# Optimization experiments

Hardware: AMD Instinct MI355X
Metric: run time of the kernel (lower is better)

Reference implementation:

```python
import jax, jax.numpy as jnp
import numpy as np

B, L, DIM, ET, NH, SD, NC = 32, 200, 36, 128, 64, 9, 2


def setup_inputs() -> dict:
    key = jax.random.key(0)
    ks = jax.random.split(key, 16)
    f = jnp.float32
    vals = jax.random.normal(ks[0], (B, L, DIM), f)
    obs = (jax.random.uniform(ks[1], (B, L, DIM)) < 0.7).astype(f)  # 0/1 observation mask
    x = jnp.concatenate([vals, obs], -1)                            # (B, L, 2*DIM)
    time_steps = jnp.sort(jax.random.uniform(ks[2], (B, L)), axis=1)
    static_info = jax.random.normal(ks[3], (B, SD), f)
    query_param = jnp.linspace(0.0, 1.0, ET, dtype=f)               # nn.Parameter(linspace)

    def lin(k, o, i, s):
        return jax.random.normal(k, (o, i), f) * s

    return dict(
        x=x, time_steps=time_steps, static_info=static_info, query_param=query_param,
        periodic_w=lin(ks[4], ET - 1, 1, 1.0), periodic_b=jnp.zeros((ET - 1,), f),
        timelin_w=lin(ks[5], 1, 1, 1.0), timelin_b=jnp.zeros((1,), f),
        qw=lin(ks[6], ET, ET, ET ** -0.5), qb=jnp.zeros((ET,), f),
        kw=lin(ks[7], ET, ET, ET ** -0.5), kb=jnp.zeros((ET,), f),
        ow=lin(ks[8], DIM, 2 * DIM, (2 * DIM) ** -0.5), ob=jnp.zeros((DIM,), f),
        gru_w_ih=lin(ks[9], 3 * NH, DIM, DIM ** -0.5),
        gru_w_hh=lin(ks[10], 3 * NH, NH, NH ** -0.5),
        gru_b_ih=jnp.zeros((3 * NH,), f), gru_b_hh=jnp.zeros((3 * NH,), f),
        st_w=lin(ks[11], 8, SD, SD ** -0.5), st_b=jnp.zeros((8,), f),
        c1_w=lin(ks[12], NH + 8, NH + 8, (NH + 8) ** -0.5), c1_b=jnp.zeros((NH + 8,), f),
        bn_g=jnp.ones((NH + 8,), f), bn_b=jnp.zeros((NH + 8,), f),
        c2_w=lin(ks[13], NC, NH + 8, (NH + 8) ** -0.5), c2_b=jnp.zeros((NC,), f),
        rand_mask=jax.random.randint(ks[14], (B, L), 0, 2, jnp.int32),
    )


def reference(x, time_steps, static_info, query_param, periodic_w, periodic_b,
              timelin_w, timelin_b, qw, qb, kw, kb, ow, ob,
              gru_w_ih, gru_w_hh, gru_b_ih, gru_b_hh, st_w, st_b,
              c1_w, c1_b, bn_g, bn_b, c2_w, c2_b, rand_mask):
    dim = x.shape[-1] // 2
    irr = x[:, :, dim:]                                   # observation mask channels
    temp = rand_mask.astype(x.dtype)[:, :, None]          # random_masking keep-mask
    m_small = irr * temp
    irr2 = jnp.concatenate([irr, irr], -1)                # (B, L, 2*dim)
    m2 = jnp.concatenate([m_small, m_small], -1)

    def time_emb(tt):
        tt = tt[..., None]
        return jnp.concatenate([tt @ timelin_w.T + timelin_b,
                                jnp.sin(tt @ periodic_w.T + periodic_b)], -1)

    key_e = time_emb(time_steps)                          # (B, L, ET)
    query_e = time_emb(query_param[None, :])[0]           # (ET, ET)
    q = query_e @ qw.T + qb                               # num_heads=1 => dk=ET
    k = key_e @ kw.T + kb
    scores = jnp.einsum('qd,bld->bql', q, k) / jnp.sqrt(jnp.asarray(ET, x.dtype))

    def mta(mask):
        # per-channel masked softmax over keys l: (B, Lq, L, 2*dim)
        s5 = jnp.where(mask[:, None, :, :] == 0, jnp.asarray(-1e9, x.dtype),
                       scores[:, :, :, None])
        p = jax.nn.softmax(s5, axis=2)
        o = jnp.einsum('bqld,bld->bqd', p, x)             # (B, Lq, 2*dim)
        return o @ ow.T + ob                              # (B, Lq, dim)

    out_te = mta(irr2)
    out1_te = mta(m2)

    sx = x[:, :, :dim]
    sx_g = jnp.round(jax.nn.sigmoid(jnp.einsum('bld,ble->bde', sx, sx)))
    sout = jax.nn.sigmoid(jnp.einsum('bqd,bqe->bde', out_te, out_te))

    def step(h, xt):  # torch GRU cell, gate order r,z,n
        gi = xt @ gru_w_ih.T + gru_b_ih
        gh = h @ gru_w_hh.T + gru_b_hh
        ir, iz, inn = jnp.split(gi, 3, -1)
        hr, hz, hn = jnp.split(gh, 3, -1)
        r = jax.nn.sigmoid(ir + hr)
        z = jax.nn.sigmoid(iz + hz)
        n = jnp.tanh(inn + r * hn)
        return (1 - z) * n + z * h, None

    h0 = jnp.zeros((x.shape[0], gru_w_hh.shape[1]), x.dtype)
    h_fin, _ = jax.lax.scan(step, h0, jnp.swapaxes(out_te, 0, 1))

    st = static_info @ st_w.T + st_b
    cls_in = jnp.concatenate([h_fin, st], 1)
    z1 = cls_in @ c1_w.T + c1_b
    mu = z1.mean(0)
    var = z1.var(0)                                       # BatchNorm1d (training stats)
    zn = (z1 - mu) / jnp.sqrt(var + 1e-5) * bn_g + bn_b
    zg = jax.nn.gelu(zn, approximate=False)
    logits = zg @ c2_w.T + c2_b
    return (out_te, out1_te, logits, sx_g, sout, query_param)
```

## Files before the change

### kernel.cpp

```cpp
#include <hip/hip_runtime.h>

#define B_   32
#define L_   200
#define DIM_ 36
#define ET_  128
#define NH_  64
#define SD_  9
#define NC_  2

#define O_TE   0
#define O_T1   147456
#define O_LG   294912
#define O_SXG  294976
#define O_SOUT 336448
#define O_QP   377920

typedef __fp16 half_t;
typedef __attribute__((ext_vector_type(2))) __fp16 half2_t;

__device__ __forceinline__ float sigm(float x) { return 1.f / (1.f + expf(-x)); }
__device__ __forceinline__ float fsigm(float x) {
  return __builtin_amdgcn_rcpf(1.f + __expf(-x));
}
__device__ __forceinline__ float ftanh(float x) {
  return 2.f * __builtin_amdgcn_rcpf(1.f + __expf(-2.f * x)) - 1.f;
}
__device__ __forceinline__ half2_t f2h2(float a, float b) {
  return __builtin_amdgcn_cvt_pkrtz(a, b);
}
__device__ __forceinline__ float dot2acc(half2_t w, half2_t h, float acc) {
#if __has_builtin(__builtin_amdgcn_fdot2)
  return __builtin_amdgcn_fdot2(w, h, acc, false);
#else
  return acc + (float)w.x * (float)h.x + (float)w.y * (float)h.y;
#endif
}

__global__ __launch_bounds__(256) void k_pre2(
    const float* __restrict__ qw, const float* __restrict__ kw,
    const float* __restrict__ qb, const float* __restrict__ qp,
    const float* __restrict__ pw, const float* __restrict__ pb,
    const float* __restrict__ tlw, const float* __restrict__ tlb,
    const float* __restrict__ x, float* __restrict__ qm2,
    float* __restrict__ xmean, float* __restrict__ out) {
  int blk = blockIdx.x, t = threadIdx.x;
  if (blk < 128) {
    __shared__ float eq[128];
    __shared__ float uq[128];
    int q = blk;
    if (t < 128) {
      float tt = qp[q];
      eq[t] = (t == 0) ? tt * tlw[0] + tlb[0]
                       : __sinf(tt * pw[t - 1] + pb[t - 1]);
    }
    __syncthreads();
    if (t < 128) {
      const float4* qw4 = (const float4*)(qw + (size_t)t * 128);
      float a = qb[t];
      #pragma unroll 8
      for (int c = 0; c < 32; c++) {
        float4 w = qw4[c];
        a += eq[4 * c] * w.x + eq[4 * c + 1] * w.y +
             eq[4 * c + 2] * w.z + eq[4 * c + 3] * w.w;
      }
      uq[t] = a;
    }
    __syncthreads();
    if (t < 128) {
      float a = 0.f;
      #pragma unroll 8
      for (int i = 0; i < 128; i++) a += uq[i] * kw[i * 128 + t];
      qm2[q * 128 + t] = a * 0.088388347648318447f;
      if (q == 0) out[O_QP + t] = qp[t];
    }
    return;
  }
  int b = blk - 128;
  if (t < 72) {
    float s = 0.f;
    const float* xb = x + (size_t)b * L_ * 72 + t;
    #pragma unroll 8
    for (int l = 0; l < L_; l++) s += xb[(size_t)l * 72];
    xmean[b * 72 + t] = s * (1.0f / L_);
  }
}

__global__ __launch_bounds__(1024, 1) void k_attn(
    const float* __restrict__ qm, const float* __restrict__ ts,
    const float* __restrict__ pw, const float* __restrict__ pb,
    const float* __restrict__ tlw, const float* __restrict__ tlb,
    const float* __restrict__ x, const int* __restrict__ rm,
    const float* __restrict__ xmean, const float* __restrict__ ow,
    const float* __restrict__ ob, float* __restrict__ out) {
  __shared__ __align__(16) char Abuf[103936];
  __shared__ __align__(16) float qs[16][128];
  __shared__ __align__(16) float sc[16][200];
  __shared__ __align__(16) float owsh[DIM_][72];
  float*   ksA  = (float*)Abuf;
  half2_t* wsh2 = (half2_t*)Abuf;
  float*   sums = (float*)(Abuf + 57600);
  float*   ofr  = (float*)(Abuf + 57600 + 36864);

  int b = blockIdx.x >> 3;
  int q0 = (blockIdx.x & 7) << 4;
  int tid = threadIdx.x;

  const float4* qsrc = (const float4*)(qm + q0 * ET_);
  for (int i = tid; i < 16 * 32; i += 1024) ((float4*)qs)[i] = qsrc[i];
  const float4* owsrc = (const float4*)ow;
  for (int i = tid; i < DIM_ * 18; i += 1024) ((float4*)owsh)[i] = owsrc[i];
  {
    float tl_w = tlw[0], tl_b = tlb[0];
    const float* tsb = ts + b * L_;
    for (int i = tid; i < L_ * 128; i += 1024) {
      int l = i >> 7, j = i & 127;
      float t = tsb[l];
      float e = (j == 0) ? t * tl_w + tl_b : __sinf(t * pw[j - 1] + pb[j - 1]);
      int blkj = (j >> 2) ^ ((l >> 2) & 7);
      ksA[(l << 7) + (blkj << 2) + (j & 3)] = e;
    }
  }
  __syncthreads();

  {
    int w = tid >> 6, lg = tid & 63;
    int qp2 = w >> 1;
    int lh = w & 1;
    float acc[2][2];
    #pragma unroll
    for (int i = 0; i < 2; i++)
      #pragma unroll
      for (int j = 0; j < 2; j++) acc[i][j] = 0.f;
    const float4* ks4 = (const float4*)ksA;
    const float4* qs4 = (const float4*)qs;
    int lbase = 100 * lh + 2 * lg;
    int swz0 = (lbase >> 2) & 7;
    int swz1 = ((lbase + 1) >> 2) & 7;
    #pragma unroll 4
    for (int d4 = 0; d4 < 32; d4++) {
      float4 kv[2];
      {
        int l0c = (lbase < 100 * lh + 100) ? lbase : (100 * lh + 99);
        int l1c = (lbase + 1 < 100 * lh + 100) ? lbase + 1 : (100 * lh + 99);
        kv[0] = ks4[(l0c << 5) + (d4 ^ swz0)];
        kv[1] = ks4[(l1c << 5) + (d4 ^ swz1)];
      }
      #pragma unroll
      for (int i = 0; i < 2; i++) {
        float4 qv = qs4[(2 * qp2 + i) * 32 + d4];
        #pragma unroll
        for (int j = 0; j < 2; j++)
          acc[i][j] += qv.x * kv[j].x + qv.y * kv[j].y +
                       qv.z * kv[j].z + qv.w * kv[j].w;
      }
    }
    if (2 * lg < 100) {
      #pragma unroll
      for (int i = 0; i < 2; i++) {
        float2 v = {acc[i][0], acc[i][1]};
        *((float2*)(&sc[2 * qp2 + i][lbase])) = v;
      }
    }
  }
  __syncthreads();

  {
    int qi = tid >> 6, li = tid & 63;
    float m = -1e30f;
    for (int l = li; l < L_; l += 64) m = fmaxf(m, sc[qi][l]);
    #pragma unroll
    for (int off = 32; off >= 1; off >>= 1) m = fmaxf(m, __shfl_xor(m, off));
    for (int l = li; l < L_; l += 64) sc[qi][l] = __expf(sc[qi][l] - m);
  }

  {
    const float2* xb2 = (const float2*)(x + (size_t)b * L_ * 72);
    const int* rmb = rm + b * L_;
    for (int i = tid; i < L_ * 72; i += 1024) {
      int l = i / 72, c2 = i % 72;
      int seg = c2 / 18, fh = c2 % 18;
      float2 v = xb2[l * 36 + fh];
      float2 o = xb2[l * 36 + 18 + fh];
      float rr = (float)rmb[l];
      float w0, w1;
      if (seg == 0)      { w0 = o.x * v.x;      w1 = o.y * v.y; }
      else if (seg == 1) { w0 = o.x;            w1 = o.y; }
      else if (seg == 2) { w0 = o.x * v.x * rr; w1 = o.y * v.y * rr; }
      else               { w0 = o.x * rr;       w1 = o.y * rr; }
      wsh2[l * 72 + c2] = f2h2(w0, w1);
    }
  }
  __syncthreads();

  {
    int quarter = tid >> 8, tt = tid & 255;
    int qi = tt >> 4, li = tt & 15;
    int l0 = quarter * 50;
    float accA[8], accB[8];
    #pragma unroll
    for (int k = 0; k < 8; k++) { accA[k] = 0.f; accB[k] = 0.f; }
    const float4* wA = (const float4*)wsh2;
    #pragma unroll 2
    for (int l = l0; l < l0 + 50; l++) {
      float ev = sc[qi][l];
      float4 wa = wA[l * 18 + li];
      union { float f; half2_t h; } u0, u1, u2, u3;
      u0.f = wa.x; u1.f = wa.y; u2.f = wa.z; u3.f = wa.w;
      accA[0] += ev * (float)u0.h.x; accA[1] += ev * (float)u0.h.y;
      accA[2] += ev * (float)u1.h.x; accA[3] += ev * (float)u1.h.y;
      accA[4] += ev * (float)u2.h.x; accA[5] += ev * (float)u2.h.y;
      accA[6] += ev * (float)u3.h.x; accA[7] += ev * (float)u3.h.y;
      if (li < 2) {
        float4 wb = wA[l * 18 + 16 + li];
        union { float f; half2_t h; } b0, b1, b2, b3;
        b0.f = wb.x; b1.f = wb.y; b2.f = wb.z; b3.f = wb.w;
        accB[0] += ev * (float)b0.h.x; accB[1] += ev * (float)b0.h.y;
        accB[2] += ev * (float)b1.h.x; accB[3] += ev * (float)b1.h.y;
        accB[4] += ev * (float)b2.h.x; accB[5] += ev * (float)b2.h.y;
        accB[6] += ev * (float)b3.h.x; accB[7] += ev * (float)b3.h.y;
      }
    }
    float* sq = sums + quarter * 2304 + qi * 144;
    float4* sA = (float4*)(sq + 8 * li);
    sA[0] = make_float4(accA[0], accA[1], accA[2], accA[3]);
    sA[1] = make_float4(accA[4], accA[5], accA[6], accA[7]);
    if (li < 2) {
      float4* sB = (float4*)(sq + 128 + 8 * li);
      sB[0] = make_float4(accB[0], accB[1], accB[2], accB[3]);
      sB[1] = make_float4(accB[4], accB[5], accB[6], accB[7]);
    }
  }
  __syncthreads();

  const float* xm = xmean + b * 72;
  for (int idx = tid; idx < 16 * DIM_; idx += 1024) {
    int qq = idx / DIM_, j = idx % DIM_;
    const float* s0 = sums + qq * 144;
    const float* s1 = s0 + 2304;
    const float* s2 = s1 + 2304;
    const float* s3 = s2 + 2304;
    float numA = (s0[j] + s1[j]) + (s2[j] + s3[j]);
    float denA = (s0[36 + j] + s1[36 + j]) + (s2[36 + j] + s3[36 + j]);
    float numB = (s0[72 + j] + s1[72 + j]) + (s2[72 + j] + s3[72 + j]);
    float denB = (s0[108 + j] + s1[108 + j]) + (s2[108 + j] + s3[108 + j]);
    float al, ah, bl, bh;
    if (denA > 0.f) { al = numA / denA; ah = 1.f; }
    else            { al = xm[j];       ah = xm[36 + j]; }
    if (denB > 0.f) { bl = numB / denB; bh = 1.f; }
    else            { bl = xm[j];       bh = xm[36 + j]; }
    float* oq = ofr + qq * 144;
    oq[j] = al;      oq[36 + j] = ah;
    oq[72 + j] = bl; oq[108 + j] = bh;
  }
  __syncthreads();

  for (int idx = tid; idx < 16 * 72; idx += 1024) {
    int qq = idx / 72, t = idx % 72;
    int v = t / DIM_, i2 = t % DIM_;
    const float4* o4 = (const float4*)(ofr + qq * 144 + v * 72);
    const float4* w4 = (const float4*)(owsh[i2]);
    float a = ob[i2];
    #pragma unroll
    for (int d4 = 0; d4 < 18; d4++) {
      float4 ov = o4[d4], wv = w4[d4];
      a += ov.x * wv.x + ov.y * wv.y + ov.z * wv.z + ov.w * wv.w;
    }
    size_t off = ((size_t)b * ET_ + q0 + qq) * DIM_ + i2;
    out[(v == 0 ? O_TE : O_T1) + off] = a;
  }
}

__global__ __launch_bounds__(256, 1) void k_sg(
    const float* __restrict__ out_ro, const float* __restrict__ x,
    const float* __restrict__ wih, const float* __restrict__ bih,
    const float* __restrict__ whh, const float* __restrict__ bhh,
    float* __restrict__ hfin, float* __restrict__ out) {
  __shared__ __align__(16) float ote_s[ET_][DIM_];
  __shared__ float gis[ET_][3 * NH_];
  __shared__ __align__(16) half2_t hpk[NH_ / 2];
  int blk = blockIdx.x, t = threadIdx.x;

  if (blk < 32) {
    int b = blk;
    float* sxs = (float*)gis;
    const float4* osrc = (const float4*)(out_ro + O_TE + (size_t)b * ET_ * DIM_);
    for (int idx = t; idx < ET_ * 9; idx += 256)
      ((float4*)&ote_s[0][0])[idx] = osrc[idx];
    const float4* xsrc = (const float4*)(x + (size_t)b * L_ * 72);
    for (int idx = t; idx < L_ * 18; idx += 256) {
      int l = idx / 18, c = idx % 18;
      ((float4*)&sxs[l * 76])[c] = xsrc[idx];
    }
    __syncthreads();
    for (int idx = t; idx < DIM_ * DIM_; idx += 256) {
      int d = idx / DIM_, e = idx % DIM_;
      float s = 0.f;
      #pragma unroll 8
      for (int q = 0; q < ET_; q++) s += ote_s[q][d] * ote_s[q][e];
      out[O_SOUT + (size_t)b * DIM_ * DIM_ + idx] = sigm(s);
    }
    for (int idx = t; idx < DIM_ * DIM_; idx += 256) {
      int d = idx / DIM_, e = idx % DIM_;
      float s = 0.f;
      #pragma unroll 8
      for (int l = 0; l < L_; l++) s += sxs[l * 76 + d] * sxs[l * 76 + e];
      out[O_SXG + (size_t)b * DIM_ * DIM_ + idx] = rintf(sigm(s));
    }
    return;
  }

  int b = blk - 32;
  const float* ote = out_ro + O_TE;
  const float4* osrc = (const float4*)(ote + (size_t)b * ET_ * DIM_);
  for (int idx = t; idx < ET_ * DIM_ / 4; idx += 256)
    ((float4*)&ote_s[0][0])[idx] = osrc[idx];
  __syncthreads();

  if (t < 3 * NH_) {
    float wv[DIM_];
    const float* wrow = wih + (size_t)t * DIM_;
    #pragma unroll
    for (int d = 0; d < DIM_; d++) wv[d] = wrow[d];
    float bi = bih[t] + ((t < 2 * NH_) ? bhh[t] : 0.f);
    for (int q = 0; q < ET_; q++) {
      const float4* xr = (const float4*)ote_s[q];
      float a = bi;
      #pragma unroll
      for (int c = 0; c < 9; c++) {
        float4 xv = xr[c];
        a += xv.x * wv[4 * c] + xv.y * wv[4 * c + 1] +
             xv.z * wv[4 * c + 2] + xv.w * wv[4 * c + 3];
      }
      gis[q][t] = a;
    }
  }
  __syncthreads();
  if (t >= 64) return;

  half2_t wr[32], wz[32], wn[32];
  {
    const float2* r0 = (const float2*)(whh + (size_t)t * NH_);
    const float2* r1 = (const float2*)(whh + (size_t)(NH_ + t) * NH_);
    const float2* r2 = (const float2*)(whh + (size_t)(2 * NH_ + t) * NH_);
    #pragma unroll
    for (int c = 0; c < 32; c++) {
      float2 a = r0[c], bb = r1[c], cc = r2[c];
      wr[c] = f2h2(a.x, a.y);
      wz[c] = f2h2(bb.x, bb.y);
      wn[c] = f2h2(cc.x, cc.y);
    }
  }
  float bh_n = bhh[2 * NH_ + t];

  float h = 0.f;
  ((half_t*)hpk)[t] = (half_t)0.f;
  for (int q = 0; q < ET_; q++) {
    float gi_r = gis[q][t];
    float gi_z = gis[q][NH_ + t];
    float gi_n = gis[q][2 * NH_ + t];
    float ar = 0.f, az = 0.f, an = 0.f;
    const float4* hp4 = (const float4*)hpk;
    #pragma unroll
    for (int c4 = 0; c4 < 8; c4++) {
      float4 hv = hp4[c4];
      union { float f; half2_t h; } u0, u1, u2, u3;
      u0.f = hv.x; u1.f = hv.y; u2.f = hv.z; u3.f = hv.w;
      int c = c4 * 4;
      ar = dot2acc(wr[c + 0], u0.h, ar);
      az = dot2acc(wz[c + 0], u0.h, az);
      an = dot2acc(wn[c + 0], u0.h, an);
      ar = dot2acc(wr[c + 1], u1.h, ar);
      az = dot2acc(wz[c + 1], u1.h, az);
      an = dot2acc(wn[c + 1], u1.h, an);
      ar = dot2acc(wr[c + 2], u2.h, ar);
      az = dot2acc(wz[c + 2], u2.h, az);
      an = dot2acc(wn[c + 2], u2.h, an);
      ar = dot2acc(wr[c + 3], u3.h, ar);
      az = dot2acc(wz[c + 3], u3.h, az);
      an = dot2acc(wn[c + 3], u3.h, an);
    }
    float r = fsigm(gi_r + ar);
    float z = fsigm(gi_z + az);
    float n = ftanh(gi_n + r * (an + bh_n));
    h = n + z * (h - n);
    ((half_t*)hpk)[t] = (half_t)h;
  }
  hfin[b * NH_ + t] = h;
}

__global__ __launch_bounds__(256) void k_cls(
    const float* __restrict__ hfin, const float* __restrict__ si,
    const float* __restrict__ stw, const float* __restrict__ stb,
    const float* __restrict__ c1w, const float* __restrict__ c1b,
    const float* __restrict__ bng, const float* __restrict__ bnb,
    const float* __restrict__ c2w, const float* __restrict__ c2b,
    float* __restrict__ out) {
  __shared__ float cin[B_][72];
  __shared__ float z1[B_][72];
  __shared__ float zg[B_][72];
  int t = threadIdx.x;
  for (int idx = t; idx < B_ * 8; idx += 256) {
    int b = idx / 8, j = idx % 8;
    float acc = stb[j];
    #pragma unroll
    for (int d = 0; d < SD_; d++) acc += si[b * SD_ + d] * stw[j * SD_ + d];
    cin[b][NH_ + j] = acc;
  }
  for (int idx = t; idx < B_ * NH_; idx += 256)
    cin[idx / NH_][idx % NH_] = hfin[idx];
  __syncthreads();
  for (int idx = t; idx < B_ * 72; idx += 256) {
    int b = idx / 72, j = idx % 72;
    float acc = c1b[j];
    #pragma unroll 8
    for (int d = 0; d < 72; d++) acc += cin[b][d] * c1w[j * 72 + d];
    z1[b][j] = acc;
  }
  __syncthreads();
  if (t < 72) {
    float mu = 0.f;
    for (int b = 0; b < B_; b++) mu += z1[b][t];
    mu *= (1.f / B_);
    float vv = 0.f;
    for (int b = 0; b < B_; b++) { float d = z1[b][t] - mu; vv += d * d; }
    vv *= (1.f / B_);
    float inv = 1.f / sqrtf(vv + 1e-5f);
    float g = bng[t], bb = bnb[t];
    for (int b = 0; b < B_; b++) {
      float zn = (z1[b][t] - mu) * inv * g + bb;
      zg[b][t] = 0.5f * zn * (1.f + erff(zn * 0.70710678118654752f));
    }
  }
  __syncthreads();
  for (int idx = t; idx < B_ * NC_; idx += 256) {
    int b = idx / NC_, c = idx % NC_;
    float acc = c2b[c];
    #pragma unroll 8
    for (int d = 0; d < 72; d++) acc += zg[b][d] * c2w[c * 72 + d];
    out[O_LG + idx] = acc;
  }
}

extern "C" void kernel_launch(void* const* d_in, const int* in_sizes, int n_in,
                              void* d_out, int out_size, void* d_ws,
                              size_t ws_size, hipStream_t stream) {
  const float* x    = (const float*)d_in[0];
  const float* ts   = (const float*)d_in[1];
  const float* si   = (const float*)d_in[2];
  const float* qp   = (const float*)d_in[3];
  const float* pw   = (const float*)d_in[4];
  const float* pb   = (const float*)d_in[5];
  const float* tlw  = (const float*)d_in[6];
  const float* tlb  = (const float*)d_in[7];
  const float* qw   = (const float*)d_in[8];
  const float* qb   = (const float*)d_in[9];
  const float* kw   = (const float*)d_in[10];
  const float* ow   = (const float*)d_in[12];
  const float* ob   = (const float*)d_in[13];
  const float* wih  = (const float*)d_in[14];
  const float* whh  = (const float*)d_in[15];
  const float* bih  = (const float*)d_in[16];
  const float* bhh  = (const float*)d_in[17];
  const float* stw  = (const float*)d_in[18];
  const float* stb  = (const float*)d_in[19];
  const float* c1w  = (const float*)d_in[20];
  const float* c1b  = (const float*)d_in[21];
  const float* bng  = (const float*)d_in[22];
  const float* bnb  = (const float*)d_in[23];
  const float* c2w  = (const float*)d_in[24];
  const float* c2b  = (const float*)d_in[25];
  const int*   rm   = (const int*)d_in[26];

  float* out = (float*)d_out;

  float* W = (float*)d_ws;
  float* ws_qm2   = W;
  float* ws_xmean = W + 16384;
  float* ws_hfin  = W + 18688;

  hipLaunchKernelGGL(k_pre2, dim3(160), dim3(256), 0, stream,
                     qw, kw, qb, qp, pw, pb, tlw, tlb, x, ws_qm2, ws_xmean,
                     out);
  hipLaunchKernelGGL(k_attn, dim3(B_ * 8), dim3(1024), 0, stream,
                     ws_qm2, ts, pw, pb, tlw, tlb, x, rm, ws_xmean, ow, ob,
                     out);
  hipLaunchKernelGGL(k_sg, dim3(64), dim3(256), 0, stream,
                     out, x, wih, bih, whh, bhh, ws_hfin, out);
  hipLaunchKernelGGL(k_cls, dim3(1), dim3(256), 0, stream,
                     ws_hfin, si, stw, stb, c1w, c1b, bng, bnb, c2w, c2b,
                     out);
}
```

Measured before the change: 231.1 us.

## Fuse attention, GRU, Gram and classifier kernels into one persistent megakernel

Result: slower. 305.2 us (+32.1%).

```diff
diff --git a/kernel.cpp b/kernel.cpp
--- a/kernel.cpp
+++ b/kernel.cpp
@@ -42,8 +42,10 @@
     const float* __restrict__ pw, const float* __restrict__ pb,
     const float* __restrict__ tlw, const float* __restrict__ tlb,
     const float* __restrict__ x, float* __restrict__ qm2,
-    float* __restrict__ xmean, float* __restrict__ out) {
+    float* __restrict__ xmean, int* __restrict__ cnt,
+    float* __restrict__ out) {
   int blk = blockIdx.x, t = threadIdx.x;
+  if (blk == 0 && t >= 128 && t < 128 + 33) cnt[t - 128] = 0;
   if (blk < 128) {
     __shared__ float eq[128];
     __shared__ float uq[128];
@@ -85,359 +87,385 @@
   }
 }
 
-__global__ __launch_bounds__(1024, 1) void k_attn(
+__global__ __launch_bounds__(1024, 1) void k_mega(
     const float* __restrict__ qm, const float* __restrict__ ts,
     const float* __restrict__ pw, const float* __restrict__ pb,
     const float* __restrict__ tlw, const float* __restrict__ tlb,
     const float* __restrict__ x, const int* __restrict__ rm,
     const float* __restrict__ xmean, const float* __restrict__ ow,
-    const float* __restrict__ ob, float* __restrict__ out) {
-  __shared__ __align__(16) char Abuf[103936];
-  __shared__ __align__(16) float qs[16][128];
-  __shared__ __align__(16) float sc[16][200];
-  __shared__ __align__(16) float owsh[DIM_][72];
-  float*   ksA  = (float*)Abuf;
-  half2_t* wsh2 = (half2_t*)Abuf;
-  float*   sums = (float*)(Abuf + 57600);
-  float*   ofr  = (float*)(Abuf + 57600 + 36864);
-
-  int b = blockIdx.x >> 3;
-  int q0 = (blockIdx.x & 7) << 4;
-  int tid = threadIdx.x;
-
-  const float4* qsrc = (const float4*)(qm + q0 * ET_);
-  for (int i = tid; i < 16 * 32; i += 1024) ((float4*)qs)[i] = qsrc[i];
-  const float4* owsrc = (const float4*)ow;
-  for (int i = tid; i < DIM_ * 18; i += 1024) ((float4*)owsh)[i] = owsrc[i];
-  {
-    float tl_w = tlw[0], tl_b = tlb[0];
-    const float* tsb = ts + b * L_;
-    for (int i = tid; i < L_ * 128; i += 1024) {
-      int l = i >> 7, j = i & 127;
-      float t = tsb[l];
-      float e = (j == 0) ? t * tl_w + tl_b : __sinf(t * pw[j - 1] + pb[j - 1]);
-      int blkj = (j >> 2) ^ ((l >> 2) & 7);
-      ksA[(l << 7) + (blkj << 2) + (j & 3)] = e;
-    }
+    const float* __restrict__ ob, const float* __restrict__ wih,
+    const float* __restrict__ bih, const float* __restrict__ whh,
+    const float* __restrict__ bhh, const float* __restrict__ si,
+    const float* __restrict__ stw, const float* __restrict__ stb,
+    const float* __restrict__ c1w, const float* __restrict__ c1b,
+    const float* __restrict__ bng, const float* __restrict__ bnb,
+    const float* __restrict__ c2w, const float* __restrict__ c2b,
+    float* __restrict__ hfin, int* __restrict__ cnt,
+    float* __restrict__ out) {
+  __shared__ __align__(16) char SMEM[135296];
+  int blk = blockIdx.x, tid = threadIdx.x;
+
+  if (blk < 256) {
+    float*   ksA  = (float*)SMEM;
+    half2_t* wsh2 = (half2_t*)SMEM;
+    float*   sums = (float*)(SMEM + 57600);
+    float*   ofr  = (float*)(SMEM + 57600 + 36864);
+    float (*qs)[128]  = (float(*)[128])(SMEM + 103936);
+    float (*sc)[200]  = (float(*)[200])(SMEM + 112128);
+    float (*owsh)[72] = (float(*)[72])(SMEM + 124928);
+
+    int b = blk >> 3;
+    int q0 = (blk & 7) << 4;
+
+    const float4* qsrc = (const float4*)(qm + q0 * ET_);
+    for (int i = tid; i < 16 * 32; i += 1024) ((float4*)qs)[i] = qsrc[i];
+    const float4* owsrc = (const float4*)ow;
+    for (int i = tid; i < DIM_ * 18; i += 1024) ((float4*)owsh)[i] = owsrc[i];
+    {
+      float tl_w = tlw[0], tl_b = tlb[0];
+      const float* tsb = ts + b * L_;
+      for (int i = tid; i < L_ * 128; i += 1024) {
+        int l = i >> 7, j = i & 127;
+        float t = tsb[l];
+        float e = (j == 0) ? t * tl_w + tl_b
+                           : __sinf(t * pw[j - 1] + pb[j - 1]);
+        int blkj = (j >> 2) ^ ((l >> 2) & 7);
+        ksA[(l << 7) + (blkj << 2) + (j & 3)] = e;
+      }
+    }
+    __syncthreads();
+
+    {
+      int w = tid >> 6, lg = tid & 63;
+      int qp2 = w >> 1, lh = w & 1;
+      float acc[2][2];
+      #pragma unroll
+      for (int i = 0; i < 2; i++)
+        #pragma unroll
+        for (int j = 0; j < 2; j++) acc[i][j] = 0.f;
+      const float4* ks4 = (const float4*)ksA;
+      const float4* qs4 = (const float4*)qs;
+      int lbase = 100 * lh + 2 * lg;
+      int swz0 = (lbase >> 2) & 7;
+      int swz1 = ((lbase + 1) >> 2) & 7;
+      #pragma unroll 4
+      for (int d4 = 0; d4 < 32; d4++) {
+        float4 kv[2];
+        {
+          int l0c = (lbase < 100 * lh + 100) ? lbase : (100 * lh + 99);
+          int l1c = (lbase + 1 < 100 * lh + 100) ? lbase + 1 : (100 * lh + 99);
+          kv[0] = ks4[(l0c << 5) + (d4 ^ swz0)];
+          kv[1] = ks4[(l1c << 5) + (d4 ^ swz1)];
+        }
+        #pragma unroll
+        for (int i = 0; i < 2; i++) {
+          float4 qv = qs4[(2 * qp2 + i) * 32 + d4];
+          #pragma unroll
+          for (int j = 0; j < 2; j++)
+            acc[i][j] += qv.x * kv[j].x + qv.y * kv[j].y +
+                         qv.z * kv[j].z + qv.w * kv[j].w;
+        }
+      }
+      if (2 * lg < 100) {
+        #pragma unroll
+        for (int i = 0; i < 2; i++) {
+          float2 v = {acc[i][0], acc[i][1]};
+          *((float2*)(&sc[2 * qp2 + i][lbase])) = v;
+        }
+      }
+    }
+    __syncthreads();
+
+    {
+      int qi = tid >> 6, li = tid & 63;
+      float m = -1e30f;
+      for (int l = li; l < L_; l += 64) m = fmaxf(m, sc[qi][l]);
+      #pragma unroll
+      for (int off = 32; off >= 1; off >>= 1) m = fmaxf(m, __shfl_xor(m, off));
+      for (int l = li; l < L_; l += 64) sc[qi][l] = __expf(sc[qi][l] - m);
+    }
+
+    {
+      const float2* xb2 = (const float2*)(x + (size_t)b * L_ * 72);
+      const int* rmb = rm + b * L_;
+      for (int i = tid; i < L_ * 72; i += 1024) {
+        int l = i / 72, c2 = i % 72;
+        int seg = c2 / 18, fh = c2 % 18;
+        float2 v = xb2[l * 36 + fh];
+        float2 o = xb2[l * 36 + 18 + fh];
+        float rr = (float)rmb[l];
+        float w0, w1;
+        if (seg == 0)      { w0 = o.x * v.x;      w1 = o.y * v.y; }
+        else if (seg == 1) { w0 = o.x;            w1 = o.y; }
+        else if (seg == 2) { w0 = o.x * v.x * rr; w1 = o.y * v.y * rr; }
+        else               { w0 = o.x * rr;       w1 = o.y * rr; }
+        wsh2[l * 72 + c2] = f2h2(w0, w1);
+      }
+    }
+    __syncthreads();
+
+    {
+      int quarter = tid >> 8, tt = tid & 255;
+      int qi = tt >> 4, li = tt & 15;
+      int l0 = quarter * 50;
+      float accA[8], accB[8];
+      #pragma unroll
+      for (int k = 0; k < 8; k++) { accA[k] = 0.f; accB[k] = 0.f; }
+      const float4* wA = (const float4*)wsh2;
+      #pragma unroll 2
+      for (int l = l0; l < l0 + 50; l++) {
+        float ev = sc[qi][l];
+        float4 wa = wA[l * 18 + li];
+        union { float f; half2_t h; } u0, u1, u2, u3;
+        u0.f = wa.x; u1.f = wa.y; u2.f = wa.z; u3.f = wa.w;
+        accA[0] += ev * (float)u0.h.x; accA[1] += ev * (float)u0.h.y;
+        accA[2] += ev * (float)u1.h.x; accA[3] += ev * (float)u1.h.y;
+        accA[4] += ev * (float)u2.h.x; accA[5] += ev * (float)u2.h.y;
+        accA[6] += ev * (float)u3.h.x; accA[7] += ev * (float)u3.h.y;
+        if (li < 2) {
+          float4 wb = wA[l * 18 + 16 + li];
+          union { float f; half2_t h; } b0, b1, b2, b3;
+          b0.f = wb.x; b1.f = wb.y; b2.f = wb.z; b3.f = wb.w;
+          accB[0] += ev * (float)b0.h.x; accB[1] += ev * (float)b0.h.y;
+          accB[2] += ev * (float)b1.h.x; accB[3] += ev * (float)b1.h.y;
+          accB[4] += ev * (float)b2.h.x; accB[5] += ev * (float)b2.h.y;
+          accB[6] += ev * (float)b3.h.x; accB[7] += ev * (float)b3.h.y;
+        }
+      }
+      float* sq = sums + quarter * 2304 + qi * 144;
+      float4* sA = (float4*)(sq + 8 * li);
+      sA[0] = make_float4(accA[0], accA[1], accA[2], accA[3]);
+      sA[1] = make_float4(accA[4], accA[5], accA[6], accA[7]);
+      if (li < 2) {
+        float4* sB = (float4*)(sq + 128 + 8 * li);
+        sB[0] = make_float4(accB[0], accB[1], accB[2], accB[3]);
+        sB[1] = make_float4(accB[4], accB[5], accB[6], accB[7]);
+      }
+    }
+    __syncthreads();
+
+    const float* xm = xmean + b * 72;
+    for (int idx = tid; idx < 16 * DIM_; idx += 1024) {
+      int qq = idx / DIM_, j = idx % DIM_;
+      const float* s0 = sums + qq * 144;
+      const float* s1 = s0 + 2304;
+      const float* s2 = s1 + 2304;
+      const float* s3 = s2 + 2304;
+      float numA = (s0[j] + s1[j]) + (s2[j] + s3[j]);
+      float denA = (s0[36 + j] + s1[36 + j]) + (s2[36 + j] + s3[36 + j]);
+      float numB = (s0[72 + j] + s1[72 + j]) + (s2[72 + j] + s3[72 + j]);
+      float denB = (s0[108 + j] + s1[108 + j]) + (s2[108 + j] + s3[108 + j]);
+      float al, ah, bl, bh;
+      if (denA > 0.f) { al = numA / denA; ah = 1.f; }
+      else            { al = xm[j];       ah = xm[36 + j]; }
+      if (denB > 0.f) { bl = numB / denB; bh = 1.f; }
+      else            { bl = xm[j];       bh = xm[36 + j]; }
+      float* oq = ofr + qq * 144;
+      oq[j] = al;      oq[36 + j] = ah;
+      oq[72 + j] = bl; oq[108 + j] = bh;
+    }
+    __syncthreads();
+
+    for (int idx = tid; idx < 16 * 72; idx += 1024) {
+      int qq = idx / 72, t = idx % 72;
+      int v = t / DIM_, i2 = t % DIM_;
+      const float4* o4 = (const float4*)(ofr + qq * 144 + v * 72);
+      const float4* w4 = (const float4*)(owsh[i2]);
+      float a = ob[i2];
+      #pragma unroll
+      for (int d4 = 0; d4 < 18; d4++) {
+        float4 ov = o4[d4], wv = w4[d4];
+        a += ov.x * wv.x + ov.y * wv.y + ov.z * wv.z + ov.w * wv.w;
+      }
+      size_t off = ((size_t)b * ET_ + q0 + qq) * DIM_ + i2;
+      out[(v == 0 ? O_TE : O_T1) + off] = a;
+    }
+    __threadfence();
+    __syncthreads();
+    if (tid == 0) atomicAdd(&cnt[b], 1);
+    return;
   }
-  __syncthreads();
-
-  {
-    int w = tid >> 6, lg = tid & 63;
-    int qp2 = w >> 1;
-    int lh = w & 1;
-    float acc[2][2];
-    #pragma unroll
-    for (int i = 0; i < 2; i++)
-      #pragma unroll
-      for (int j = 0; j < 2; j++) acc[i][j] = 0.f;
-    const float4* ks4 = (const float4*)ksA;
-    const float4* qs4 = (const float4*)qs;
-    int lbase = 100 * lh + 2 * lg;
-    int swz0 = (lbase >> 2) & 7;
-    int swz1 = ((lbase + 1) >> 2) & 7;
-    #pragma unroll 4
-    for (int d4 = 0; d4 < 32; d4++) {
-      float4 kv[2];
-      {
-        int l0c = (lbase < 100 * lh + 100) ? lbase : (100 * lh + 99);
-        int l1c = (lbase + 1 < 100 * lh + 100) ? lbase + 1 : (100 * lh + 99);
-        kv[0] = ks4[(l0c << 5) + (d4 ^ swz0)];
-        kv[1] = ks4[(l1c << 5) + (d4 ^ swz1)];
-      }
-      #pragma unroll
-      for (int i = 0; i < 2; i++) {
-        float4 qv = qs4[(2 * qp2 + i) * 32 + d4];
+
+  if (blk < 288) {
+    int b = blk - 256;
+    float (*ote_s)[DIM_] = (float(*)[DIM_])SMEM;
+    float (*gis)[3 * NH_] = (float(*)[3 * NH_])(SMEM + 18432);
+    half2_t* hpk = (half2_t*)(SMEM + 116736);
+    if (tid == 0) {
+      while (atomicAdd(&cnt[b], 0) < 8) { }
+    }
+    __syncthreads();
+    __threadfence();
+
+    const float* ote = out + O_TE;
+    const float4* osrc = (const float4*)(ote + (size_t)b * ET_ * DIM_);
+    for (int idx = tid; idx < ET_ * DIM_ / 4; idx += 1024)
+      ((float4*)&ote_s[0][0])[idx] = osrc[idx];
+    __syncthreads();
+
+    if (tid < 768) {
+      int tt = tid % 192, qg = tid / 192;
+      float wv[DIM_];
+      const float* wrow = wih + (size_t)tt * DIM_;
+      #pragma unroll
+      for (int d = 0; d < DIM_; d++) wv[d] = wrow[d];
+      float bi = bih[tt] + ((tt < 2 * NH_) ? bhh[tt] : 0.f);
+      for (int q = 32 * qg; q < 32 * qg + 32; q++) {
+        const float4* xr = (const float4*)ote_s[q];
+        float a = bi;
         #pragma unroll
-        for (int j = 0; j < 2; j++)
-          acc[i][j] += qv.x * kv[j].x + qv.y * kv[j].y +
-                       qv.z * kv[j].z + qv.w * kv[j].w;
-      }
-    }
-    if (2 * lg < 100) {
-      #pragma unroll
-      for (int i = 0; i < 2; i++) {
-        float2 v = {acc[i][0], acc[i][1]};
-        *((float2*)(&sc[2 * qp2 + i][lbase])) = v;
-      }
-    }
+        for (int c = 0; c < 9; c++) {
+          float4 xv = xr[c];
+          a += xv.x * wv[4 * c] + xv.y * wv[4 * c + 1] +
+               xv.z * wv[4 * c + 2] + xv.w * wv[4 * c + 3];
+        }
+        gis[q][tt] = a;
+      }
+    }
+    __syncthreads();
+    if (tid >= 64) return;
+    int t = tid;
+
+    half2_t wr[32], wz[32], wn[32];
+    {
+      const float2* r0 = (const float2*)(whh + (size_t)t * NH_);
+      const float2* r1 = (const float2*)(whh + (size_t)(NH_ + t) * NH_);
+      const float2* r2 = (const float2*)(whh + (size_t)(2 * NH_ + t) * NH_);
+      #pragma unroll
+      for (int c = 0; c < 32; c++) {
+        float2 a = r0[c], bb = r1[c], cc = r2[c];
+        wr[c] = f2h2(a.x, a.y);
+        wz[c] = f2h2(bb.x, bb.y);
+        wn[c] = f2h2(cc.x, cc.y);
+      }
+    }
+    float bh_n = bhh[2 * NH_ + t];
+
+    float h = 0.f;
+    ((half_t*)hpk)[t] = (half_t)0.f;
+    for (int q = 0; q < ET_; q++) {
+      float gi_r = gis[q][t];
+      float gi_z = gis[q][NH_ + t];
+      float gi_n = gis[q][2 * NH_ + t];
+      float ar = 0.f, az = 0.f, an = 0.f;
+      const float4* hp4 = (const float4*)hpk;
+      #pragma unroll
+      for (int c4 = 0; c4 < 8; c4++) {
+        float4 hv = hp4[c4];
+        union { float f; half2_t h; } u0, u1, u2, u3;
+        u0.f = hv.x; u1.f = hv.y; u2.f = hv.z; u3.f = hv.w;
+        int c = c4 * 4;
+        ar = dot2acc(wr[c + 0], u0.h, ar);
+        az = dot2acc(wz[c + 0], u0.h, az);
+        an = dot2acc(wn[c + 0], u0.h, an);
+        ar = dot2acc(wr[c + 1], u1.h, ar);
+        az = dot2acc(wz[c + 1], u1.h, az);
+        an = dot2acc(wn[c + 1], u1.h, an);
+        ar = dot2acc(wr[c + 2], u2.h, ar);
+        az = dot2acc(wz[c + 2], u2.h, az);
+        an = dot2acc(wn[c + 2], u2.h, an);
+        ar = dot2acc(wr[c + 3], u3.h, ar);
+        az = dot2acc(wz[c + 3], u3.h, az);
+        an = dot2acc(wn[c + 3], u3.h, an);
+      }
+      float r = fsigm(gi_r + ar);
+      float z = fsigm(gi_z + az);
+      float n = ftanh(gi_n + r * (an + bh_n));
+      h = n + z * (h - n);
+      ((half_t*)hpk)[t] = (half_t)h;
+    }
+    hfin[b * NH_ + t] = h;
+    __threadfence();
+    if (t == 0) atomicAdd(&cnt[32], 1);
+    return;
   }
-  __syncthreads();
-
-  {
-    int qi = tid >> 6, li = tid & 63;
-    float m = -1e30f;
-    for (int l = li; l < L_; l += 64) m = fmaxf(m, sc[qi][l]);
-    #pragma unroll
-    for (int off = 32; off >= 1; off >>= 1) m = fmaxf(m, __shfl_xor(m, off));
-    for (int l = li; l < L_; l += 64) sc[qi][l] = __expf(sc[qi][l] - m);
-  }
-
-  {
-    const float2* xb2 = (const float2*)(x + (size_t)b * L_ * 72);
-    const int* rmb = rm + b * L_;
-    for (int i = tid; i < L_ * 72; i += 1024) {
-      int l = i / 72, c2 = i % 72;
-      int seg = c2 / 18, fh = c2 % 18;
-      float2 v = xb2[l * 36 + fh];
-      float2 o = xb2[l * 36 + 18 + fh];
-      float rr = (float)rmb[l];
-      float w0, w1;
-      if (seg == 0)      { w0 = o.x * v.x;      w1 = o.y * v.y; }
-      else if (seg == 1) { w0 = o.x;            w1 = o.y; }
-      else if (seg == 2) { w0 = o.x * v.x * rr; w1 = o.y * v.y * rr; }
-      else               { w0 = o.x * rr;       w1 = o.y * rr; }
-      wsh2[l * 72 + c2] = f2h2(w0, w1);
-    }
-  }
-  __syncthreads();
-
-  {
-    int quarter = tid >> 8, tt = tid & 255;
-    int qi = tt >> 4, li = tt & 15;
-    int l0 = quarter * 50;
-    float accA[8], accB[8];
-    #pragma unroll
-    for (int k = 0; k < 8; k++) { accA[k] = 0.f; accB[k] = 0.f; }
-    const float4* wA = (const float4*)wsh2;
-    #pragma unroll 2
-    for (int l = l0; l < l0 + 50; l++) {
-      float ev = sc[qi][l];
-      float4 wa = wA[l * 18 + li];
-      union { float f; half2_t h; } u0, u1, u2, u3;
-      u0.f = wa.x; u1.f = wa.y; u2.f = wa.z; u3.f = wa.w;
-      accA[0] += ev * (float)u0.h.x; accA[1] += ev * (float)u0.h.y;
-      accA[2] += ev * (float)u1.h.x; accA[3] += ev * (float)u1.h.y;
-      accA[4] += ev * (float)u2.h.x; accA[5] += ev * (float)u2.h.y;
-      accA[6] += ev * (float)u3.h.x; accA[7] += ev * (float)u3.h.y;
-      if (li < 2) {
-        float4 wb = wA[l * 18 + 16 + li];
-        union { float f; half2_t h; } b0, b1, b2, b3;
-        b0.f = wb.x; b1.f = wb.y; b2.f = wb.z; b3.f = wb.w;
-        accB[0] += ev * (float)b0.h.x; accB[1] += ev * (float)b0.h.y;
-        accB[2] += ev * (float)b1.h.x; accB[3] += ev * (float)b1.h.y;
-        accB[4] += ev * (float)b2.h.x; accB[5] += ev * (float)b2.h.y;
-        accB[6] += ev * (float)b3.h.x; accB[7] += ev * (float)b3.h.y;
-      }
-    }
-    float* sq = sums + quarter * 2304 + qi * 144;
-    float4* sA = (float4*)(sq + 8 * li);
-    sA[0] = make_float4(accA[0], accA[1], accA[2], accA[3]);
-    sA[1] = make_float4(accA[4], accA[5], accA[6], accA[7]);
-    if (li < 2) {
-      float4* sB = (float4*)(sq + 128 + 8 * li);
-      sB[0] = make_float4(accB[0], accB[1], accB[2], accB[3]);
-      sB[1] = make_float4(accB[4], accB[5], accB[6], accB[7]);
-    }
-  }
-  __syncthreads();
-
-  const float* xm = xmean + b * 72;
-  for (int idx = tid; idx < 16 * DIM_; idx += 1024) {
-    int qq = idx / DIM_, j = idx % DIM_;
-    const float* s0 = sums + qq * 144;
-    const float* s1 = s0 + 2304;
-    const float* s2 = s1 + 2304;
-    const float* s3 = s2 + 2304;
-    float numA = (s0[j] + s1[j]) + (s2[j] + s3[j]);
-    float denA = (s0[36 + j] + s1[36 + j]) + (s2[36 + j] + s3[36 + j]);
-    float numB = (s0[72 + j] + s1[72 + j]) + (s2[72 + j] + s3[72 + j]);
-    float denB = (s0[108 + j] + s1[108 + j]) + (s2[108 + j] + s3[108 + j]);
-    float al, ah, bl, bh;
-    if (denA > 0.f) { al = numA / denA; ah = 1.f; }
-    else            { al = xm[j];       ah = xm[36 + j]; }
-    if (denB > 0.f) { bl = numB / denB; bh = 1.f; }
-    else            { bl = xm[j];       bh = xm[36 + j]; }
-    float* oq = ofr + qq * 144;
-    oq[j] = al;      oq[36 + j] = ah;
-    oq[72 + j] = bl; oq[108 + j] = bh;
-  }
-  __syncthreads();
-
-  for (int idx = tid; idx < 16 * 72; idx += 1024) {
-    int qq = idx / 72, t = idx % 72;
-    int v = t / DIM_, i2 = t % DIM_;
-    const float4* o4 = (const float4*)(ofr + qq * 144 + v * 72);
-    const float4* w4 = (const float4*)(owsh[i2]);
-    float a = ob[i2];
-    #pragma unroll
-    for (int d4 = 0; d4 < 18; d4++) {
-      float4 ov = o4[d4], wv = w4[d4];
-      a += ov.x * wv.x + ov.y * wv.y + ov.z * wv.z + ov.w * wv.w;
-    }
-    size_t off = ((size_t)b * ET_ + q0 + qq) * DIM_ + i2;
-    out[(v == 0 ? O_TE : O_T1) + off] = a;
-  }
-}
-
-__global__ __launch_bounds__(256, 1) void k_sg(
-    const float* __restrict__ out_ro, const float* __restrict__ x,
-    const float* __restrict__ wih, const float* __restrict__ bih,
-    const float* __restrict__ whh, const float* __restrict__ bhh,
-    float* __restrict__ hfin, float* __restrict__ out) {
-  __shared__ __align__(16) float ote_s[ET_][DIM_];
-  __shared__ float gis[ET_][3 * NH_];
-  __shared__ __align__(16) half2_t hpk[NH_ / 2];
-  int blk = blockIdx.x, t = threadIdx.x;
-
-  if (blk < 32) {
-    int b = blk;
-    float* sxs = (float*)gis;
-    const float4* osrc = (const float4*)(out_ro + O_TE + (size_t)b * ET_ * DIM_);
-    for (int idx = t; idx < ET_ * 9; idx += 256)
-      ((float4*)&ote_s[0][0])[idx] = osrc[idx];
+
+  if (blk < 320) {
+    int b = blk - 288;
+    float (*ote_s)[DIM_] = (float(*)[DIM_])SMEM;
+    float* sxs = (float*)(SMEM + 18432);
     const float4* xsrc = (const float4*)(x + (size_t)b * L_ * 72);
-    for (int idx = t; idx < L_ * 18; idx += 256) {
+    for (int idx = tid; idx < L_ * 18; idx += 1024) {
       int l = idx / 18, c = idx % 18;
       ((float4*)&sxs[l * 76])[c] = xsrc[idx];
     }
     __syncthreads();
-    for (int idx = t; idx < DIM_ * DIM_; idx += 256) {
+    for (int idx = tid; idx < DIM_ * DIM_; idx += 1024) {
+      int d = idx / DIM_, e = idx % DIM_;
+      float s = 0.f;
+      #pragma unroll 8
+      for (int l = 0; l < L_; l++) s += sxs[l * 76 + d] * sxs[l * 76 + e];
+      out[O_SXG + (size_t)b * DIM_ * DIM_ + idx] = rintf(sigm(s));
+    }
+    if (tid == 0) {
+      while (atomicAdd(&cnt[b], 0) < 8) { }
+    }
+    __syncthreads();
+    __threadfence();
+    const float4* osrc = (const float4*)(out + O_TE + (size_t)b * ET_ * DIM_);
+    for (int idx = tid; idx < ET_ * 9; idx += 1024)
+      ((float4*)&ote_s[0][0])[idx] = osrc[idx];
+    __syncthreads();
+    for (int idx = tid; idx < DIM_ * DIM_; idx += 1024) {
       int d = idx / DIM_, e = idx % DIM_;
       float s = 0.f;
       #pragma unroll 8
       for (int q = 0; q < ET_; q++) s += ote_s[q][d] * ote_s[q][e];
       out[O_SOUT + (size_t)b * DIM_ * DIM_ + idx] = sigm(s);
     }
-    for (int idx = t; idx < DIM_ * DIM_; idx += 256) {
-      int d = idx / DIM_, e = idx % DIM_;
-      float s = 0.f;
-      #pragma unroll 8
-      for (int l = 0; l < L_; l++) s += sxs[l * 76 + d] * sxs[l * 76 + e];
-      out[O_SXG + (size_t)b * DIM_ * DIM_ + idx] = rintf(sigm(s));
-    }
     return;
   }
 
-  int b = blk - 32;
-  const float* ote = out_ro + O_TE;
-  const float4* osrc = (const float4*)(ote + (size_t)b * ET_ * DIM_);
-  for (int idx = t; idx < ET_ * DIM_ / 4; idx += 256)
-    ((float4*)&ote_s[0][0])[idx] = osrc[idx];
-  __syncthreads();
-
-  if (t < 3 * NH_) {
-    float wv[DIM_];
-    const float* wrow = wih + (size_t)t * DIM_;
-    #pragma unroll
-    for (int d = 0; d < DIM_; d++) wv[d] = wrow[d];
-    float bi = bih[t] + ((t < 2 * NH_) ? bhh[t] : 0.f);
-    for (int q = 0; q < ET_; q++) {
-      const float4* xr = (const float4*)ote_s[q];
-      float a = bi;
-      #pragma unroll
-      for (int c = 0; c < 9; c++) {
-        float4 xv = xr[c];
-        a += xv.x * wv[4 * c] + xv.y * wv[4 * c + 1] +
-             xv.z * wv[4 * c + 2] + xv.w * wv[4 * c + 3];
-      }
-      gis[q][t] = a;
-    }
-  }
-  __syncthreads();
-  if (t >= 64) return;
-
-  half2_t wr[32], wz[32], wn[32];
   {
-    const float2* r0 = (const float2*)(whh + (size_t)t * NH_);
-    const float2* r1 = (const float2*)(whh + (size_t)(NH_ + t) * NH_);
-    const float2* r2 = (const float2*)(whh + (size_t)(2 * NH_ + t) * NH_);
-    #pragma unroll
-    for (int c = 0; c < 32; c++) {
-      float2 a = r0[c], bb = r1[c], cc = r2[c];
-      wr[c] = f2h2(a.x, a.y);
-      wz[c] = f2h2(bb.x, bb.y);
-      wn[c] = f2h2(cc.x, cc.y);
-    }
-  }
-  float bh_n = bhh[2 * NH_ + t];
-
-  float h = 0.f;
-  ((half_t*)hpk)[t] = (half_t)0.f;
-  for (int q = 0; q < ET_; q++) {
-    float gi_r = gis[q][t];
-    float gi_z = gis[q][NH_ + t];
-    float gi_n = gis[q][2 * NH_ + t];
-    float ar = 0.f, az = 0.f, an = 0.f;
-    const float4* hp4 = (const float4*)hpk;
-    #pragma unroll
-    for (int c4 = 0; c4 < 8; c4++) {
-      float4 hv = hp4[c4];
-      union { float f; half2_t h; } u0, u1, u2, u3;
-      u0.f = hv.x; u1.f = hv.y; u2.f = hv.z; u3.f = hv.w;
-      int c = c4 * 4;
-      ar = dot2acc(wr[c + 0], u0.h, ar);
-      az = dot2acc(wz[c + 0], u0.h, az);
-      an = dot2acc(wn[c + 0], u0.h, an);
-      ar = dot2acc(wr[c + 1], u1.h, ar);
-      az = dot2acc(wz[c + 1], u1.h, az);
-      an = dot2acc(wn[c + 1], u1.h, an);
-      ar = dot2acc(wr[c + 2], u2.h, ar);
-      az = dot2acc(wz[c + 2], u2.h, az);
-      an = dot2acc(wn[c + 2], u2.h, an);
-      ar = dot2acc(wr[c + 3], u3.h, ar);
-      az = dot2acc(wz[c + 3], u3.h, az);
-      an = dot2acc(wn[c + 3], u3.h, an);
-    }
-    float r = fsigm(gi_r + ar);
-    float z = fsigm(gi_z + az);
-    float n = ftanh(gi_n + r * (an + bh_n));
-    h = n + z * (h - n);
-    ((half_t*)hpk)[t] = (half_t)h;
-  }
-  hfin[b * NH_ + t] = h;
-}
-
-__global__ __launch_bounds__(256) void k_cls(
-    const float* __restrict__ hfin, const float* __restrict__ si,
-    const float* __restrict__ stw, const float* __restrict__ stb,
-    const float* __restrict__ c1w, const float* __restrict__ c1b,
-    const float* __restrict__ bng, const float* __restrict__ bnb,
-    const float* __restrict__ c2w, const float* __restrict__ c2b,
-    float* __restrict__ out) {
-  __shared__ float cin[B_][72];
-  __shared__ float z1[B_][72];
-  __shared__ float zg[B_][72];
-  int t = threadIdx.x;
-  for (int idx = t; idx < B_ * 8; idx += 256) {
-    int b = idx / 8, j = idx % 8;
-    float acc = stb[j];
-    #pragma unroll
-    for (int d = 0; d < SD_; d++) acc += si[b * SD_ + d] * stw[j * SD_ + d];
-    cin[b][NH_ + j] = acc;
-  }
-  for (int idx = t; idx < B_ * NH_; idx += 256)
-    cin[idx / NH_][idx % NH_] = hfin[idx];
-  __syncthreads();
-  for (int idx = t; idx < B_ * 72; idx += 256) {
-    int b = idx / 72, j = idx % 72;
-    float acc = c1b[j];
-    #pragma unroll 8
-    for (int d = 0; d < 72; d++) acc += cin[b][d] * c1w[j * 72 + d];
-    z1[b][j] = acc;
-  }
-  __syncthreads();
-  if (t < 72) {
-    float mu = 0.f;
-    for (int b = 0; b < B_; b++) mu += z1[b][t];
-    mu *= (1.f / B_);
-    float vv = 0.f;
-    for (int b = 0; b < B_; b++) { float d = z1[b][t] - mu; vv += d * d; }
-    vv *= (1.f / B_);
-    float inv = 1.f / sqrtf(vv + 1e-5f);
-    float g = bng[t], bb = bnb[t];
-    for (int b = 0; b < B_; b++) {
-      float zn = (z1[b][t] - mu) * inv * g + bb;
-      zg[b][t] = 0.5f * zn * (1.f + erff(zn * 0.70710678118654752f));
-    }
-  }
-  __syncthreads();
-  for (int idx = t; idx < B_ * NC_; idx += 256) {
-    int b = idx / NC_, c = idx % NC_;
-    float acc = c2b[c];
-    #pragma unroll 8
-    for (int d = 0; d < 72; d++) acc += zg[b][d] * c2w[c * 72 + d];
-    out[O_LG + idx] = acc;
+    float (*cin)[72] = (float(*)[72])SMEM;
+    float (*z1)[72]  = (float(*)[72])(SMEM + 9216);
+    float (*zg)[72]  = (float(*)[72])(SMEM + 18432);
+    if (tid == 0) {
+      while (atomicAdd(&cnt[32], 0) < 32) { }
+    }
+    __syncthreads();
+    __threadfence();
+    int t = tid;
+    for (int idx = t; idx < B_ * 8; idx += 1024) {
+      int b = idx / 8, j = idx % 8;
+      float acc = stb[j];
+      #pragma unroll
+      for (int d = 0; d < SD_; d++) acc += si[b * SD_ + d] * stw[j * SD_ + d];
+      cin[b][NH_ + j] = acc;
+    }
+    for (int idx = t; idx < B_ * NH_; idx += 1024)
+      cin[idx / NH_][idx % NH_] = hfin[idx];
+    __syncthreads();
+    for (int idx = t; idx < B_ * 72; idx += 1024) {
+      int b = idx / 72, j = idx % 72;
+      float acc = c1b[j];
+      #pragma unroll 8
+      for (int d = 0; d < 72; d++) acc += cin[b][d] * c1w[j * 72 + d];
+      z1[b][j] = acc;
+    }
+    __syncthreads();
+    if (t < 72) {
+      float mu = 0.f;
+      for (int b = 0; b < B_; b++) mu += z1[b][t];
+      mu *= (1.f / B_);
+      float vv = 0.f;
+      for (int b = 0; b < B_; b++) { float d = z1[b][t] - mu; vv += d * d; }
+      vv *= (1.f / B_);
+      float inv = 1.f / sqrtf(vv + 1e-5f);
+      float g = bng[t], bb = bnb[t];
+      for (int b = 0; b < B_; b++) {
+        float zn = (z1[b][t] - mu) * inv * g + bb;
+        zg[b][t] = 0.5f * zn * (1.f + erff(zn * 0.70710678118654752f));
+      }
+    }
+    __syncthreads();
+    for (int idx = t; idx < B_ * NC_; idx += 1024) {
+      int b = idx / NC_, c = idx % NC_;
+      float acc = c2b[c];
+      #pragma unroll 8
+      for (int d = 0; d < 72; d++) acc += zg[b][d] * c2w[c * 72 + d];
+      out[O_LG + idx] = acc;
+    }
   }
 }
 
@@ -477,16 +505,13 @@
   float* ws_qm2   = W;
   float* ws_xmean = W + 16384;
   float* ws_hfin  = W + 18688;
+  int*   ws_cnt   = (int*)(W + 20736);
 
   hipLaunchKernelGGL(k_pre2, dim3(160), dim3(256), 0, stream,
                      qw, kw, qb, qp, pw, pb, tlw, tlb, x, ws_qm2, ws_xmean,
-                     out);
-  hipLaunchKernelGGL(k_attn, dim3(B_ * 8), dim3(1024), 0, stream,
+                     ws_cnt, out);
+  hipLaunchKernelGGL(k_mega, dim3(321), dim3(1024), 0, stream,
                      ws_qm2, ts, pw, pb, tlw, tlb, x, rm, ws_xmean, ow, ob,
-                     out);
-  hipLaunchKernelGGL(k_sg, dim3(64), dim3(256), 0, stream,
-                     out, x, wih, bih, whh, bhh, ws_hfin, out);
-  hipLaunchKernelGGL(k_cls, dim3(1), dim3(256), 0, stream,
-                     ws_hfin, si, stw, stb, c1w, c1b, bng, bnb, c2w, c2b,
-                     out);
-}
+                     wih, bih, whh, bhh, si, stw, stb, c1w, c1b, bng, bnb,
+                     c2w, c2b, ws_hfin, ws_cnt, out);
+}
```
